# Optimization experiments

Measured on AMD Instinct MI355X. Metric: run time of the kernel, lower is better.

Reference implementation:

```python
import jax, jax.numpy as jnp
import numpy as np

SEQ_LEN = 256
NLAYERS = 3
H = 128  # latent_dim == input_dim
OUT_DIM = 2
BATCH = 1024


def setup_inputs() -> dict:
    key = jax.random.key(0)
    ks = jax.random.split(key, 7)
    s = 1.0 / np.sqrt(H)  # PyTorch RNN init scale
    return {
        "hiddens": jax.random.normal(ks[0], (BATCH, NLAYERS, H), jnp.float32),
        "W_ih": jax.random.uniform(ks[1], (NLAYERS, 3 * H, H), jnp.float32, -s, s),
        "W_hh": jax.random.uniform(ks[2], (NLAYERS, 3 * H, H), jnp.float32, -s, s),
        "b_ih": jax.random.uniform(ks[3], (NLAYERS, 3 * H), jnp.float32, -s, s),
        "b_hh": jax.random.uniform(ks[4], (NLAYERS, 3 * H), jnp.float32, -s, s),
        "fc_w": jax.random.uniform(ks[5], (OUT_DIM, H), jnp.float32, -s, s),
        "fc_b": jax.random.uniform(ks[6], (OUT_DIM,), jnp.float32, -s, s),
    }


def _gru_cell(x, h, w_ih, w_hh, bi, bh):
    # x, h: [B, H]; w_*: [3H, H]; b_*: [3H]; PyTorch gate order (r, z, n)
    gx = x @ w_ih.T + bi          # [B, 3H]
    gh = h @ w_hh.T + bh          # [B, 3H]
    xr, xz, xn = jnp.split(gx, 3, axis=-1)
    hr, hz, hn = jnp.split(gh, 3, axis=-1)
    r = jax.nn.sigmoid(xr + hr)
    z = jax.nn.sigmoid(xz + hz)
    n = jnp.tanh(xn + r * hn)
    return (1.0 - z) * n + z * h


def reference(hiddens, W_ih, W_hh, b_ih, b_hh, fc_w, fc_b):
    # hiddens: [B, L, H] -> layer-major [L, B, H] (torch transposes 0,1)
    h = jnp.transpose(hiddens, (1, 0, 2))
    B = hiddens.shape[0]
    x0 = jnp.zeros((B, H), hiddens.dtype)  # torch.zeros initial input

    def step(carry, _):
        x, h = carry
        new_h = []
        inp = x
        for l in range(NLAYERS):
            hl = _gru_cell(inp, h[l], W_ih[l], W_hh[l], b_ih[l], b_hh[l])
            new_h.append(hl)
            inp = hl  # top-layer output feeds next layer / next step
        return (inp, jnp.stack(new_h)), inp

    (_, _), outs = jax.lax.scan(step, (x0, h), None, length=SEQ_LEN)
    outs = jnp.transpose(outs, (1, 0, 2))        # [B, T, H]
    return outs @ fc_w.T + fc_b                  # [B, T, out_dim]
```

## Files before the change

kernel.cpp:

```cpp
#include <hip/hip_runtime.h>
#include <stdint.h>

typedef int   v4i __attribute__((ext_vector_type(4)));
typedef float v4f __attribute__((ext_vector_type(4)));

#define SLOT_SZ  12288
#define LO_OFF   6144
#define BIAS_OFF (2*SLOT_SZ)
#define FC_OFF   (BIAS_OFF + 6144)
#define SMEM_SZ  (FC_OFF + 2048)

#define QW   1436.84056f
#define C1f  4.38394754e-5f
#define C2f  3.45193507e-7f
#define L2E  1.44269504f
#define CR1  (-(L2E)*C1f)
#define CR2  (-(L2E)*C2f)
#define CX1  (2.0f*L2E*C1f)
#define CX2  (2.0f*L2E*C2f)

#define MFMA(A,B,C) __builtin_amdgcn_mfma_i32_16x16x64_i8(A, B, C, 0, 0, 0)

__global__ void prep_weights(const float* __restrict__ Wih,
                             const float* __restrict__ Whh,
                             int8_t* __restrict__ img) {
  int bid = blockIdx.x, lane = threadIdx.x;
  int w = bid / 36, blk = bid % 36;
  int l = blk / 12, rem = blk % 12, o = rem >> 1, kh = rem & 1;
  const float* M = (o & 1) ? Whh : Wih;
  int row = (o >> 1) * 128 + w * 16 + (lane & 15);
  int k0 = kh * 64 + (lane >> 4) * 16;
  const float* src = M + l * 49152 + row * 128 + k0;
  int words[4];
  #pragma unroll
  for (int j4 = 0; j4 < 4; ++j4) {
    unsigned wd = 0;
    #pragma unroll
    for (int j = 0; j < 4; ++j) {
      int q = (int)rintf(src[j4 * 4 + j] * QW);
      wd |= ((unsigned)(q & 255)) << (8 * j);
    }
    words[j4] = (int)wd;
  }
  *(v4i*)(img + (((long)bid) * 64 + lane) * 16) = *(const v4i*)words;
}

#define DECL6(S) v4i S##Rh=z4,S##Rl=z4,S##Zh=z4,S##Zl=z4,S##Hh=z4,S##Hl=z4
#define ZERO6(S) do{S##Rh=z4;S##Rl=z4;S##Zh=z4;S##Zl=z4;S##Hh=z4;S##Hl=z4;}while(0)

#define HMFMA_B(S,L,H0,LL0,H1,LL1) do { \
  S##Rh = MFMA(wr[(L)*12+2],  H0, S##Rh);  S##Rl = MFMA(wr[(L)*12+2],  LL0, S##Rl); \
  S##Zh = MFMA(wr[(L)*12+6],  H0, S##Zh);  S##Zl = MFMA(wr[(L)*12+6],  LL0, S##Zl); \
  S##Hh = MFMA(wr[(L)*12+10], H0, S##Hh);  S##Hl = MFMA(wr[(L)*12+10], LL0, S##Hl); \
  S##Rh = MFMA(wr[(L)*12+3],  H1, S##Rh);  S##Rl = MFMA(wr[(L)*12+3],  LL1, S##Rl); \
  S##Zh = MFMA(wr[(L)*12+7],  H1, S##Zh);  S##Zl = MFMA(wr[(L)*12+7],  LL1, S##Zl); \
  S##Hh = MFMA(wr[(L)*12+11], H1, S##Hh);  S##Hl = MFMA(wr[(L)*12+11], LL1, S##Hl); \
} while(0)

#define XMFMA_C(S,L,X0,XL0,X1,XL1) do { \
  S##Rh = MFMA(wr[(L)*12+0], X0, S##Rh);  S##Rl = MFMA(wr[(L)*12+0], XL0, S##Rl); \
  S##Zh = MFMA(wr[(L)*12+4], X0, S##Zh);  S##Zl = MFMA(wr[(L)*12+4], XL0, S##Zl); \
  Xh    = MFMA(wr[(L)*12+8], X0, Xh);     Xl    = MFMA(wr[(L)*12+8], XL0, Xl); \
  S##Rh = MFMA(wr[(L)*12+1], X1, S##Rh);  S##Rl = MFMA(wr[(L)*12+1], XL1, S##Rl); \
  S##Zh = MFMA(wr[(L)*12+5], X1, S##Zh);  S##Zl = MFMA(wr[(L)*12+5], XL1, S##Zl); \
  Xh    = MFMA(wr[(L)*12+9], X1, Xh);     Xl    = MFMA(wr[(L)*12+9], XL1, Xl); \
} while(0)

#define EW6(S, L, SN) do { \
  v4f bRv = *(const v4f*)(biasb + ((L)*4 + 0) * 512); \
  v4f bZv = *(const v4f*)(biasb + ((L)*4 + 1) * 512); \
  v4f bXv = *(const v4f*)(biasb + ((L)*4 + 2) * 512); \
  v4f bHv = *(const v4f*)(biasb + ((L)*4 + 3) * 512); \
  int hi_i[4], lo_i[4]; \
  _Pragma("unroll") \
  for (int r = 0; r < 4; ++r) { \
    float gR = fmaf(CR1, (float)S##Rh[r], fmaf(CR2, (float)S##Rl[r], bRv[r])); \
    float gZ = fmaf(CR1, (float)S##Zh[r], fmaf(CR2, (float)S##Zl[r], bZv[r])); \
    float gX = fmaf(CX1, (float)Xh[r],    fmaf(CX2, (float)Xl[r],    bXv[r])); \
    float gH = fmaf(CX1, (float)S##Hh[r], fmaf(CX2, (float)S##Hl[r], bHv[r])); \
    float rg = __builtin_amdgcn_rcpf(1.f + __builtin_amdgcn_exp2f(gR)); \
    float zg = __builtin_amdgcn_rcpf(1.f + __builtin_amdgcn_exp2f(gZ)); \
    float u  = __builtin_amdgcn_rcpf(1.f + __builtin_amdgcn_exp2f(fmaf(rg, gH, gX))); \
    float ng = fmaf(-2.f, u, 1.f); \
    float hn = fmaf(zg, hst[L][r] - ng, ng); \
    hst[L][r] = hn; \
    float f = hn * 15.875f, fhi = rintf(f); \
    hi_i[r] = (int)fhi; \
    lo_i[r] = (int)rintf((f - fhi) * 127.f); \
  } \
  unsigned ph01 = __builtin_amdgcn_perm((unsigned)hi_i[1], (unsigned)hi_i[0], 0x00000400u); \
  unsigned ph23 = __builtin_amdgcn_perm((unsigned)hi_i[3], (unsigned)hi_i[2], 0x04000000u); \
  unsigned hiw  = __builtin_amdgcn_perm(ph23, ph01, 0x07060100u); \
  unsigned pl01 = __builtin_amdgcn_perm((unsigned)lo_i[1], (unsigned)lo_i[0], 0x00000400u); \
  unsigned pl23 = __builtin_amdgcn_perm((unsigned)lo_i[3], (unsigned)lo_i[2], 0x04000000u); \
  unsigned low  = __builtin_amdgcn_perm(pl23, pl01, 0x07060100u); \
  *(unsigned*)(ewb + (SN) + (L)*2048)          = hiw; \
  *(unsigned*)(ewb + (SN) + (L)*2048 + LO_OFF) = low; \
} while(0)

#define LOADF(D0,D1,D2,D3, OFF) \
  D0 = *(const v4i*)(fragb + (OFF)); \
  D1 = *(const v4i*)(fragb + (OFF) + LO_OFF); \
  D2 = *(const v4i*)(fragb + (OFF) + 1024); \
  D3 = *(const v4i*)(fragb + (OFF) + 1024 + LO_OFF);

#define PHASE(CS, BS, L, LB, XOFF, HOFF, SN) do { \
  v4i xh0,xl0,xh1,xl1, hh0,hl0,hh1,hl1; \
  LOADF(xh0,xl0,xh1,xl1, XOFF) \
  LOADF(hh0,hl0,hh1,hl1, HOFF) \
  ZERO6(BS); \
  HMFMA_B(BS, LB, hh0,hl0,hh1,hl1); \
  Xh = z4; Xl = z4; \
  XMFMA_C(CS, L, xh0,xl0,xh1,xl1); \
  EW6(CS, L, SN); \
  __syncthreads(); \
} while(0)

#define PHASE_L0(CS, BS, XOFF, HOFF, SN, TIDX, GUARD) do { \
  v4i xh0,xl0,xh1,xl1, hh0,hl0,hh1,hl1; \
  LOADF(xh0,xl0,xh1,xl1, XOFF) \
  LOADF(hh0,hl0,hh1,hl1, HOFF) \
  ZERO6(BS); \
  HMFMA_B(BS, 1, hh0,hl0,hh1,hl1); \
  Xh = z4; Xl = z4; \
  if (GUARD) { \
    XMFMA_C(CS, 0, xh0,xl0,xh1,xl1); \
    if (w == 0) { \
      v4i dh = z4, dl = z4; \
      v4i fwA = *(const v4i*)(smem + FC_OFF + 0 * 1024 + lane * 16); \
      v4i fwB = *(const v4i*)(smem + FC_OFF + 1 * 1024 + lane * 16); \
      dh = MFMA(fwA, xh0, dh);  dl = MFMA(fwA, xl0, dl); \
      dh = MFMA(fwB, xh1, dh);  dl = MFMA(fwB, xl1, dl); \
      if (q == 0) { \
        float2 o2; \
        o2.x = fcb0 + C1f * (float)dh[0] + C2f * (float)dl[0]; \
        o2.y = fcb1 + C1f * (float)dh[1] + C2f * (float)dl[1]; \
        *(float2*)(out + (((long)(wg * 16 + col)) * 256 + (TIDX)) * 2) = o2; \
      } \
    } \
  } \
  EW6(CS, 0, SN); \
  __syncthreads(); \
} while(0)

__global__ __launch_bounds__(512, 1)
void gru_main(const float* __restrict__ hiddens, const float* __restrict__ bih,
              const float* __restrict__ bhh, const float* __restrict__ fcw,
              const float* __restrict__ fcb, const int8_t* __restrict__ img,
              float* __restrict__ out) {
  extern __shared__ char smem[];
  const int tid = threadIdx.x, wg = blockIdx.x;
  const int lane = tid & 63, w = tid >> 6, col = lane & 15, q = lane >> 4;
  const v4i z4 = {0, 0, 0, 0};

  v4i wr[36];
  #pragma unroll
  for (int i = 0; i < 36; ++i)
    wr[i] = *(const v4i*)(img + (((long)(w * 36 + i)) * 64 + lane) * 16);

  if (tid < 128) {
    int kh = tid >> 6, ln = tid & 63, c2 = ln & 15, q2 = ln >> 4;
    int words[4] = {0, 0, 0, 0};
    if (c2 < 2) {
      const float* src = fcw + c2 * 128 + kh * 64 + q2 * 16;
      #pragma unroll
      for (int j4 = 0; j4 < 4; ++j4) {
        unsigned wd = 0;
        #pragma unroll
        for (int j = 0; j < 4; ++j) {
          int qv = (int)rintf(src[j4 * 4 + j] * QW);
          wd |= ((unsigned)(qv & 255)) << (8 * j);
        }
        words[j4] = (int)wd;
      }
    }
    *(v4i*)(smem + FC_OFF + kh * 1024 + ln * 16) = *(const v4i*)words;
  }
  for (int i = tid; i < 1536; i += 512) {
    int l = i >> 9, type = (i >> 7) & 3, h = i & 127;
    float bv;
    if      (type == 0) bv = -L2E * (bih[l * 384 + h]       + bhh[l * 384 + h]);
    else if (type == 1) bv = -L2E * (bih[l * 384 + 128 + h] + bhh[l * 384 + 128 + h]);
    else if (type == 2) bv = 2.0f * L2E * bih[l * 384 + 256 + h];
    else                bv = 2.0f * L2E * bhh[l * 384 + 256 + h];
    *(float*)(smem + BIAS_OFF + i * 4) = bv;
  }
  for (int i = tid; i < 6144; i += 512) {
    int l = i >> 11, b = (i >> 7) & 15, h = i & 127;
    float v = hiddens[((long)(wg * 16 + b)) * 384 + l * 128 + h];
    float f = v * 15.875f, fhi = rintf(f);
    int addr = l * 2048 + (h >> 4) * 256 + b * 16 + (h & 15);
    *(int8_t*)(smem + addr)          = (int8_t)(int)fhi;
    *(int8_t*)(smem + addr + LO_OFF) = (int8_t)(int)rintf((f - fhi) * 127.f);
  }
  v4f hst[3];
  #pragma unroll
  for (int l = 0; l < 3; ++l)
    #pragma unroll
    for (int r = 0; r < 4; ++r)
      hst[l][r] = hiddens[((long)(wg * 16 + col)) * 384 + l * 128 + w * 16 + q * 4 + r];

  const float fcb0 = fcb[0], fcb1 = fcb[1];
  __syncthreads();

  const char* fragb = smem + lane * 16;
  char* ewb = smem + w * 256 + col * 16 + q * 4;
  const char* biasb = smem + BIAS_OFF + (w * 16 + q * 4) * 4;

  DECL6(P);
  DECL6(Q);
  v4i Xh, Xl;

  {
    v4i hh0, hl0, hh1, hl1;
    LOADF(hh0, hl0, hh1, hl1, 0)
    HMFMA_B(P, 0, hh0, hl0, hh1, hl1);
  }

  #pragma unroll 1
  for (int t = 0; t < 256; t += 2) {
    PHASE_L0(P, Q, 0 + 2 * 2048,       0 + 2048,           SLOT_SZ, t - 1, (t > 0));
    PHASE   (Q, P, 1, 2, SLOT_SZ + 0,        0 + 2 * 2048,       SLOT_SZ);
    PHASE   (P, Q, 2, 0, SLOT_SZ + 2048,     SLOT_SZ + 0,        SLOT_SZ);
    PHASE_L0(Q, P, SLOT_SZ + 2 * 2048, SLOT_SZ + 2048,     0,       t,     1);
    PHASE   (P, Q, 1, 2, 0 + 0,              SLOT_SZ + 2 * 2048, 0);
    PHASE   (Q, P, 2, 0, 0 + 2048,           0 + 0,              0);
  }
  if (w == 0) {
    v4i dh = z4, dl = z4;
    v4i xh0 = *(const v4i*)(fragb + 2 * 2048);
    v4i xl0 = *(const v4i*)(fragb + 2 * 2048 + LO_OFF);
    v4i xh1 = *(const v4i*)(fragb + 2 * 2048 + 1024);
    v4i xl1 = *(const v4i*)(fragb + 2 * 2048 + 1024 + LO_OFF);
    v4i fwA = *(const v4i*)(smem + FC_OFF + 0 * 1024 + lane * 16);
    v4i fwB = *(const v4i*)(smem + FC_OFF + 1 * 1024 + lane * 16);
    dh = MFMA(fwA, xh0, dh);  dl = MFMA(fwA, xl0, dl);
    dh = MFMA(fwB, xh1, dh);  dl = MFMA(fwB, xl1, dl);
    if (q == 0) {
      float2 o2;
      o2.x = fcb0 + C1f * (float)dh[0] + C2f * (float)dl[0];
      o2.y = fcb1 + C1f * (float)dh[1] + C2f * (float)dl[1];
      *(float2*)(out + (((long)(wg * 16 + col)) * 256 + 255) * 2) = o2;
    }
  }
}

extern "C" void kernel_launch(void* const* d_in, const int* in_sizes, int n_in,
                              void* d_out, int out_size, void* d_ws, size_t ws_size,
                              hipStream_t stream) {
  (void)in_sizes; (void)n_in; (void)out_size; (void)ws_size;
  const float* hiddens = (const float*)d_in[0];
  const float* Wih     = (const float*)d_in[1];
  const float* Whh     = (const float*)d_in[2];
  const float* bih     = (const float*)d_in[3];
  const float* bhh     = (const float*)d_in[4];
  const float* fcw     = (const float*)d_in[5];
  const float* fcb     = (const float*)d_in[6];
  int8_t* img = (int8_t*)d_ws;
  float* out = (float*)d_out;

  prep_weights<<<288, 64, 0, stream>>>(Wih, Whh, img);
  gru_main<<<64, 512, SMEM_SZ, stream>>>(hiddens, bih, bhh, fcw, fcb, img, out);
}
```

Measured before the change: 785.0 us.

## Carry layer inputs in registers across phases and drop cross-phase accumulator pipelining

Restructures the recurrent step so each layer phase computes its hidden and input MFMAs back to back into fresh accumulators. Previously the hidden-side MFMAs for the next layer were issued early into a second accumulator set. Previous-step hidden fragments are now kept in registers (A/B/C) instead of being reloaded from shared memory, and the first MFMA of each chain takes the zero accumulator directly instead of zeroing registers. This cuts LDS reloads and accumulator register pressure. In exchange it gives up the cross-phase overlap of hidden MFMAs with the elementwise tail and sync.

```diff
diff --git a/kernel.cpp b/kernel.cpp
--- a/kernel.cpp
+++ b/kernel.cpp
@@ -45,28 +45,36 @@
   *(v4i*)(img + (((long)bid) * 64 + lane) * 16) = *(const v4i*)words;
 }
 
-#define DECL6(S) v4i S##Rh=z4,S##Rl=z4,S##Zh=z4,S##Zl=z4,S##Hh=z4,S##Hl=z4
-#define ZERO6(S) do{S##Rh=z4;S##Rl=z4;S##Zh=z4;S##Zl=z4;S##Hh=z4;S##Hl=z4;}while(0)
-
-#define HMFMA_B(S,L,H0,LL0,H1,LL1) do { \
-  S##Rh = MFMA(wr[(L)*12+2],  H0, S##Rh);  S##Rl = MFMA(wr[(L)*12+2],  LL0, S##Rl); \
-  S##Zh = MFMA(wr[(L)*12+6],  H0, S##Zh);  S##Zl = MFMA(wr[(L)*12+6],  LL0, S##Zl); \
-  S##Hh = MFMA(wr[(L)*12+10], H0, S##Hh);  S##Hl = MFMA(wr[(L)*12+10], LL0, S##Hl); \
-  S##Rh = MFMA(wr[(L)*12+3],  H1, S##Rh);  S##Rl = MFMA(wr[(L)*12+3],  LL1, S##Rl); \
-  S##Zh = MFMA(wr[(L)*12+7],  H1, S##Zh);  S##Zl = MFMA(wr[(L)*12+7],  LL1, S##Zl); \
-  S##Hh = MFMA(wr[(L)*12+11], H1, S##Hh);  S##Hl = MFMA(wr[(L)*12+11], LL1, S##Hl); \
-} while(0)
-
-#define XMFMA_C(S,L,X0,XL0,X1,XL1) do { \
-  S##Rh = MFMA(wr[(L)*12+0], X0, S##Rh);  S##Rl = MFMA(wr[(L)*12+0], XL0, S##Rl); \
-  S##Zh = MFMA(wr[(L)*12+4], X0, S##Zh);  S##Zl = MFMA(wr[(L)*12+4], XL0, S##Zl); \
-  Xh    = MFMA(wr[(L)*12+8], X0, Xh);     Xl    = MFMA(wr[(L)*12+8], XL0, Xl); \
-  S##Rh = MFMA(wr[(L)*12+1], X1, S##Rh);  S##Rl = MFMA(wr[(L)*12+1], XL1, S##Rl); \
-  S##Zh = MFMA(wr[(L)*12+5], X1, S##Zh);  S##Zl = MFMA(wr[(L)*12+5], XL1, S##Zl); \
-  Xh    = MFMA(wr[(L)*12+9], X1, Xh);     Xl    = MFMA(wr[(L)*12+9], XL1, Xl); \
-} while(0)
-
-#define EW6(S, L, SN) do { \
+#define DECL_ACC v4i aRh, aRl, aZh, aZl, aXh, aXl, aHh, aHl
+
+#define HMFMA_Z(L,H0,LL0,H1,LL1) do { \
+  aRh = MFMA(wr[(L)*12+2],  H0,  zacc);  aRl = MFMA(wr[(L)*12+2],  LL0, zacc); \
+  aZh = MFMA(wr[(L)*12+6],  H0,  zacc);  aZl = MFMA(wr[(L)*12+6],  LL0, zacc); \
+  aHh = MFMA(wr[(L)*12+10], H0,  zacc);  aHl = MFMA(wr[(L)*12+10], LL0, zacc); \
+  aRh = MFMA(wr[(L)*12+3],  H1,  aRh);   aRl = MFMA(wr[(L)*12+3],  LL1, aRl); \
+  aZh = MFMA(wr[(L)*12+7],  H1,  aZh);   aZl = MFMA(wr[(L)*12+7],  LL1, aZl); \
+  aHh = MFMA(wr[(L)*12+11], H1,  aHh);   aHl = MFMA(wr[(L)*12+11], LL1, aHl); \
+} while(0)
+
+#define XMFMA(L,X0,XL0,X1,XL1) do { \
+  aRh = MFMA(wr[(L)*12+0], X0,  aRh);  aRl = MFMA(wr[(L)*12+0], XL0, aRl); \
+  aZh = MFMA(wr[(L)*12+4], X0,  aZh);  aZl = MFMA(wr[(L)*12+4], XL0, aZl); \
+  aXh = MFMA(wr[(L)*12+8], X0,  aXh);  aXl = MFMA(wr[(L)*12+8], XL0, aXl); \
+  aRh = MFMA(wr[(L)*12+1], X1,  aRh);  aRl = MFMA(wr[(L)*12+1], XL1, aRl); \
+  aZh = MFMA(wr[(L)*12+5], X1,  aZh);  aZl = MFMA(wr[(L)*12+5], XL1, aZl); \
+  aXh = MFMA(wr[(L)*12+9], X1,  aXh);  aXl = MFMA(wr[(L)*12+9], XL1, aXl); \
+} while(0)
+
+#define XMFMA_Z(L,X0,XL0,X1,XL1) do { \
+  aRh = MFMA(wr[(L)*12+0], X0,  aRh);   aRl = MFMA(wr[(L)*12+0], XL0, aRl); \
+  aZh = MFMA(wr[(L)*12+4], X0,  aZh);   aZl = MFMA(wr[(L)*12+4], XL0, aZl); \
+  aXh = MFMA(wr[(L)*12+8], X0,  zacc);  aXl = MFMA(wr[(L)*12+8], XL0, zacc); \
+  aRh = MFMA(wr[(L)*12+1], X1,  aRh);   aRl = MFMA(wr[(L)*12+1], XL1, aRl); \
+  aZh = MFMA(wr[(L)*12+5], X1,  aZh);   aZl = MFMA(wr[(L)*12+5], XL1, aZl); \
+  aXh = MFMA(wr[(L)*12+9], X1,  aXh);   aXl = MFMA(wr[(L)*12+9], XL1, aXl); \
+} while(0)
+
+#define EW_WRITE(L, SN) do { \
   v4f bRv = *(const v4f*)(biasb + ((L)*4 + 0) * 512); \
   v4f bZv = *(const v4f*)(biasb + ((L)*4 + 1) * 512); \
   v4f bXv = *(const v4f*)(biasb + ((L)*4 + 2) * 512); \
@@ -74,10 +82,10 @@
   int hi_i[4], lo_i[4]; \
   _Pragma("unroll") \
   for (int r = 0; r < 4; ++r) { \
-    float gR = fmaf(CR1, (float)S##Rh[r], fmaf(CR2, (float)S##Rl[r], bRv[r])); \
-    float gZ = fmaf(CR1, (float)S##Zh[r], fmaf(CR2, (float)S##Zl[r], bZv[r])); \
-    float gX = fmaf(CX1, (float)Xh[r],    fmaf(CX2, (float)Xl[r],    bXv[r])); \
-    float gH = fmaf(CX1, (float)S##Hh[r], fmaf(CX2, (float)S##Hl[r], bHv[r])); \
+    float gR = fmaf(CR1, (float)aRh[r], fmaf(CR2, (float)aRl[r], bRv[r])); \
+    float gZ = fmaf(CR1, (float)aZh[r], fmaf(CR2, (float)aZl[r], bZv[r])); \
+    float gX = fmaf(CX1, (float)aXh[r], fmaf(CX2, (float)aXl[r], bXv[r])); \
+    float gH = fmaf(CX1, (float)aHh[r], fmaf(CX2, (float)aHl[r], bHv[r])); \
     float rg = __builtin_amdgcn_rcpf(1.f + __builtin_amdgcn_exp2f(gR)); \
     float zg = __builtin_amdgcn_rcpf(1.f + __builtin_amdgcn_exp2f(gZ)); \
     float u  = __builtin_amdgcn_rcpf(1.f + __builtin_amdgcn_exp2f(fmaf(rg, gH, gX))); \
@@ -98,49 +106,53 @@
   *(unsigned*)(ewb + (SN) + (L)*2048 + LO_OFF) = low; \
 } while(0)
 
-#define LOADF(D0,D1,D2,D3, OFF) \
-  D0 = *(const v4i*)(fragb + (OFF)); \
-  D1 = *(const v4i*)(fragb + (OFF) + LO_OFF); \
-  D2 = *(const v4i*)(fragb + (OFF) + 1024); \
-  D3 = *(const v4i*)(fragb + (OFF) + 1024 + LO_OFF);
-
-#define PHASE(CS, BS, L, LB, XOFF, HOFF, SN) do { \
-  v4i xh0,xl0,xh1,xl1, hh0,hl0,hh1,hl1; \
-  LOADF(xh0,xl0,xh1,xl1, XOFF) \
-  LOADF(hh0,hl0,hh1,hl1, HOFF) \
-  ZERO6(BS); \
-  HMFMA_B(BS, LB, hh0,hl0,hh1,hl1); \
-  Xh = z4; Xl = z4; \
-  XMFMA_C(CS, L, xh0,xl0,xh1,xl1); \
-  EW6(CS, L, SN); \
-  __syncthreads(); \
-} while(0)
-
-#define PHASE_L0(CS, BS, XOFF, HOFF, SN, TIDX, GUARD) do { \
-  v4i xh0,xl0,xh1,xl1, hh0,hl0,hh1,hl1; \
-  LOADF(xh0,xl0,xh1,xl1, XOFF) \
-  LOADF(hh0,hl0,hh1,hl1, HOFF) \
-  ZERO6(BS); \
-  HMFMA_B(BS, 1, hh0,hl0,hh1,hl1); \
-  Xh = z4; Xl = z4; \
-  if (GUARD) { \
-    XMFMA_C(CS, 0, xh0,xl0,xh1,xl1); \
-    if (w == 0) { \
-      v4i dh = z4, dl = z4; \
-      v4i fwA = *(const v4i*)(smem + FC_OFF + 0 * 1024 + lane * 16); \
-      v4i fwB = *(const v4i*)(smem + FC_OFF + 1 * 1024 + lane * 16); \
-      dh = MFMA(fwA, xh0, dh);  dl = MFMA(fwA, xl0, dl); \
-      dh = MFMA(fwB, xh1, dh);  dl = MFMA(fwB, xl1, dl); \
-      if (q == 0) { \
-        float2 o2; \
-        o2.x = fcb0 + C1f * (float)dh[0] + C2f * (float)dl[0]; \
-        o2.y = fcb1 + C1f * (float)dh[1] + C2f * (float)dl[1]; \
-        *(float2*)(out + (((long)(wg * 16 + col)) * 256 + (TIDX)) * 2) = o2; \
+#define STEP(SO, SN, FCIDX, FCGUARD) do { \
+  { DECL_ACC; \
+    aXh = zacc; aXl = zacc; \
+    Ch0 = *(const v4i*)(fragb + (SO) + 2*2048); \
+    Cl0 = *(const v4i*)(fragb + (SO) + 2*2048 + LO_OFF); \
+    Ch1 = *(const v4i*)(fragb + (SO) + 2*2048 + 1024); \
+    Cl1 = *(const v4i*)(fragb + (SO) + 2*2048 + 1024 + LO_OFF); \
+    HMFMA_Z(0, Ah0, Al0, Ah1, Al1); \
+    if (FCGUARD) { \
+      XMFMA(0, Ch0, Cl0, Ch1, Cl1); \
+      if (w == 0) { \
+        v4i fwA = *(const v4i*)(smem + FC_OFF + 0*1024 + lane*16); \
+        v4i fwB = *(const v4i*)(smem + FC_OFF + 1*1024 + lane*16); \
+        v4i dh = MFMA(fwA, Ch0, zacc); \
+        v4i dl = MFMA(fwA, Cl0, zacc); \
+        dh = MFMA(fwB, Ch1, dh);  dl = MFMA(fwB, Cl1, dl); \
+        if (q == 0) { \
+          float2 o2; \
+          o2.x = fcb0 + C1f*(float)dh[0] + C2f*(float)dl[0]; \
+          o2.y = fcb1 + C1f*(float)dh[1] + C2f*(float)dl[1]; \
+          *(float2*)(out + (((long)(wg*16+col))*256 + (FCIDX))*2) = o2; \
+        } \
       } \
     } \
-  } \
-  EW6(CS, 0, SN); \
-  __syncthreads(); \
+    EW_WRITE(0, SN); \
+    __syncthreads(); \
+  } \
+  { DECL_ACC; \
+    Ah0 = *(const v4i*)(fragb + (SN) + 0); \
+    Al0 = *(const v4i*)(fragb + (SN) + 0 + LO_OFF); \
+    Ah1 = *(const v4i*)(fragb + (SN) + 1024); \
+    Al1 = *(const v4i*)(fragb + (SN) + 1024 + LO_OFF); \
+    HMFMA_Z(1, Bh0, Bl0, Bh1, Bl1); \
+    XMFMA_Z(1, Ah0, Al0, Ah1, Al1); \
+    EW_WRITE(1, SN); \
+    __syncthreads(); \
+  } \
+  { DECL_ACC; \
+    Bh0 = *(const v4i*)(fragb + (SN) + 2048); \
+    Bl0 = *(const v4i*)(fragb + (SN) + 2048 + LO_OFF); \
+    Bh1 = *(const v4i*)(fragb + (SN) + 2048 + 1024); \
+    Bl1 = *(const v4i*)(fragb + (SN) + 2048 + 1024 + LO_OFF); \
+    HMFMA_Z(2, Ch0, Cl0, Ch1, Cl1); \
+    XMFMA_Z(2, Bh0, Bl0, Bh1, Bl1); \
+    EW_WRITE(2, SN); \
+    __syncthreads(); \
+  } \
 } while(0)
 
 __global__ __launch_bounds__(512, 1)
@@ -151,7 +163,7 @@
   extern __shared__ char smem[];
   const int tid = threadIdx.x, wg = blockIdx.x;
   const int lane = tid & 63, w = tid >> 6, col = lane & 15, q = lane >> 4;
-  const v4i z4 = {0, 0, 0, 0};
+  const v4i zacc = {0, 0, 0, 0};
 
   v4i wr[36];
   #pragma unroll
@@ -207,34 +219,30 @@
   char* ewb = smem + w * 256 + col * 16 + q * 4;
   const char* biasb = smem + BIAS_OFF + (w * 16 + q * 4) * 4;
 
-  DECL6(P);
-  DECL6(Q);
-  v4i Xh, Xl;
-
-  {
-    v4i hh0, hl0, hh1, hl1;
-    LOADF(hh0, hl0, hh1, hl1, 0)
-    HMFMA_B(P, 0, hh0, hl0, hh1, hl1);
-  }
+  v4i Ah0 = *(const v4i*)(fragb + 0);
+  v4i Al0 = *(const v4i*)(fragb + 0 + LO_OFF);
+  v4i Ah1 = *(const v4i*)(fragb + 1024);
+  v4i Al1 = *(const v4i*)(fragb + 1024 + LO_OFF);
+  v4i Bh0 = *(const v4i*)(fragb + 2048);
+  v4i Bl0 = *(const v4i*)(fragb + 2048 + LO_OFF);
+  v4i Bh1 = *(const v4i*)(fragb + 2048 + 1024);
+  v4i Bl1 = *(const v4i*)(fragb + 2048 + 1024 + LO_OFF);
+  v4i Ch0, Cl0, Ch1, Cl1;
 
   #pragma unroll 1
   for (int t = 0; t < 256; t += 2) {
-    PHASE_L0(P, Q, 0 + 2 * 2048,       0 + 2048,           SLOT_SZ, t - 1, (t > 0));
-    PHASE   (Q, P, 1, 2, SLOT_SZ + 0,        0 + 2 * 2048,       SLOT_SZ);
-    PHASE   (P, Q, 2, 0, SLOT_SZ + 2048,     SLOT_SZ + 0,        SLOT_SZ);
-    PHASE_L0(Q, P, SLOT_SZ + 2 * 2048, SLOT_SZ + 2048,     0,       t,     1);
-    PHASE   (P, Q, 1, 2, 0 + 0,              SLOT_SZ + 2 * 2048, 0);
-    PHASE   (Q, P, 2, 0, 0 + 2048,           0 + 0,              0);
+    STEP(0,       SLOT_SZ, t - 1, (t > 0));
+    STEP(SLOT_SZ, 0,       t,     1);
   }
   if (w == 0) {
-    v4i dh = z4, dl = z4;
     v4i xh0 = *(const v4i*)(fragb + 2 * 2048);
     v4i xl0 = *(const v4i*)(fragb + 2 * 2048 + LO_OFF);
     v4i xh1 = *(const v4i*)(fragb + 2 * 2048 + 1024);
     v4i xl1 = *(const v4i*)(fragb + 2 * 2048 + 1024 + LO_OFF);
     v4i fwA = *(const v4i*)(smem + FC_OFF + 0 * 1024 + lane * 16);
     v4i fwB = *(const v4i*)(smem + FC_OFF + 1 * 1024 + lane * 16);
-    dh = MFMA(fwA, xh0, dh);  dl = MFMA(fwA, xl0, dl);
+    v4i dh = MFMA(fwA, xh0, zacc);
+    v4i dl = MFMA(fwA, xl0, zacc);
     dh = MFMA(fwB, xh1, dh);  dl = MFMA(fwB, xl1, dl);
     if (q == 0) {
       float2 o2;
```

New measurement: 772.6 us. No clear change (-1.6%).
